# Kernel optimization log

Measured on AMD Instinct MI355X. Metric: run time of the kernel, lower is better.

## Reference

```python
import jax, jax.numpy as jnp
import numpy as np

# Sizes
N, T, P, D = 1000, 4, 10, 13          # nodes, point types, edge types (T*(T+1)/2), basis dim per point
F, H, EA, K, E = 128, 128, 16, 64, 20000  # node feat, edge hidden, edge attr/feat, edge op bottleneck, edges
I_NODE = D * (D + 1) // 2             # 91: symmetric ('ij=ji') self-block irreps dim
I_EDGE = D * D                        # 169: generic ('ij') block irreps dim
AVG_NEIGH = 20.0


def setup_inputs() -> dict:
    ks = jax.random.split(jax.random.key(0), 16)
    Fin = H + 2 * F                   # edge-op input: [edge_msg, node_h_i, node_h_j]
    return {
        'node_feats': jax.random.normal(ks[0], (N, F), jnp.float32),
        'node_attrs': jax.random.uniform(ks[1], (N, T), dtype=jnp.float32),
        'edge_feats': jax.random.normal(ks[2], (E, EA), jnp.float32),
        'edge_attrs': jax.random.normal(ks[3], (E, EA), jnp.float32),
        'edge_index': jax.random.randint(ks[4], (2, E), 0, N),
        'node_types': jax.random.randint(ks[5], (N,), 0, T),
        'edge_types': jax.random.randint(ks[6], (E,), 0, P),
        'W_msg': jax.random.normal(ks[7], (F, F), jnp.float32) / np.float32(np.sqrt(F)),
        'W_attr': jax.random.normal(ks[8], (T, F), jnp.float32) / np.float32(np.sqrt(T)),
        'W_em': jax.random.normal(ks[9], (2 * F + 2 * EA, H), jnp.float32) / np.float32(np.sqrt(2 * F + 2 * EA)),
        'W_proj': jax.random.normal(ks[10], (Fin, K), jnp.float32) / np.float32(np.sqrt(Fin)),
        'W_node': jax.random.normal(ks[11], (T, F, I_NODE), jnp.float32) / np.float32(np.sqrt(F)),
        'W_edge': jax.random.normal(ks[12], (P, K, I_EDGE), jnp.float32) / np.float32(np.sqrt(K)),
        'cob_node': jax.random.normal(ks[13], (T, I_NODE, D, D), jnp.float32) / np.float32(D),
        'cob_edge': jax.random.normal(ks[14], (P, I_EDGE, D, D), jnp.float32) / np.float32(D),
    }


def reference(node_feats, node_attrs, edge_feats, edge_attrs, edge_index, node_types,
              edge_types, W_msg, W_attr, W_em, W_proj, W_node, W_edge, cob_node, cob_edge):
    src, dst = edge_index[0], edge_index[1]
    # --- node message passing (NodeMessageBlock, simplified linear-aggregate form) ---
    m = node_feats @ W_msg                                             # [N, F]
    agg = jax.ops.segment_sum(m[src], dst, num_segments=N) \
        + jax.ops.segment_sum(m[dst], src, num_segments=N)             # symmetric edge list: both dirs
    node_h = node_feats + agg / AVG_NEIGH + node_attrs @ W_attr        # [N, F]
    # --- edge messages (EdgeMessageBlock, simplified) ---
    e_in = jnp.concatenate([node_h[src], node_h[dst], edge_feats, edge_attrs], axis=-1)
    edge_msg = jnp.tanh(e_in @ W_em)                                   # [E, H]
    # --- self-interaction blocks: per-type gather -> op -> einsum('ni,ixy->nxy', ., cob) ---
    node_irred = jnp.einsum('nf,nfi->ni', node_h, W_node[node_types])  # [N, I_NODE]
    node_blocks = jnp.einsum('ni,nixy->nxy', node_irred, cob_node[node_types])  # [N, D, D]
    # --- interaction blocks: per-edge-type op + change of basis, transpose-symmetrized ---
    onehot = jax.nn.one_hot(edge_types, P, dtype=node_feats.dtype)     # [E, P] type selector

    def edge_block(a, b):
        h = jnp.concatenate([edge_msg, a, b], axis=-1) @ W_proj        # [E, K]
        irr = jnp.einsum('epi,ep->ei', jnp.einsum('ek,pki->epi', h, W_edge), onehot)  # [E, I_EDGE]
        return jnp.einsum('epxy,ep->exy', jnp.einsum('ei,pixy->epxy', irr, cob_edge), onehot)  # [E, D, D]

    blk_ij = edge_block(node_h[src], node_h[dst])
    blk_ji = edge_block(node_h[dst], node_h[src])
    edge_blocks = 0.5 * (blk_ij + jnp.swapaxes(blk_ji, -1, -2))        # symm_transpose
    # --- scatter blocks into the dense symmetric block matrix ---
    off = jnp.arange(D)
    nidx = jnp.arange(N)[:, None] * D + off                            # [N, D] diagonal block rows/cols
    rs = src[:, None] * D + off                                        # [E, D]
    cs = dst[:, None] * D + off
    M = jnp.zeros((N * D, N * D), node_feats.dtype)
    M = M.at[nidx[:, :, None], nidx[:, None, :]].add(node_blocks)
    M = M.at[rs[:, :, None], cs[:, None, :]].add(edge_blocks)
    M = M.at[cs[:, :, None], rs[:, None, :]].add(jnp.swapaxes(edge_blocks, -1, -2))
    return M
```

## Files before the change

### kernel.cpp

```cpp
#include <hip/hip_runtime.h>
#include <cmath>

#define NN   1000
#define TT   4
#define PP   10
#define DD   13
#define FF   128
#define HH   128
#define EAA  16
#define KDIM 64
#define EE   20000
#define I_NODE 91
#define I_EDGE 169
#define MROW  13000

__global__ __launch_bounds__(256) void k_zero(float4* __restrict__ p, long n4) {
  long i = (long)blockIdx.x * 256 + threadIdx.x;
  if (i < n4) p[i] = make_float4(0.f, 0.f, 0.f, 0.f);
}

__global__ __launch_bounds__(192) void k_comb_edge(
    const float* __restrict__ We, const float* __restrict__ cob,
    float* __restrict__ Wcomb) {
  int pk = blockIdx.x;
  int p = pk >> 6;
  int t = threadIdx.x;
  if (t >= I_EDGE) return;
  float acc = 0.f;
  const float* wrow = We + pk * I_EDGE;
  const float* crow = cob + p * I_EDGE * I_EDGE + t;
  for (int i = 0; i < I_EDGE; ++i) acc += wrow[i] * crow[i * I_EDGE];
  Wcomb[pk * I_EDGE + t] = acc;
}

__global__ __launch_bounds__(192) void k_comb_node(
    const float* __restrict__ Wn, const float* __restrict__ cob,
    float* __restrict__ Wnc) {
  int tf = blockIdx.x;
  int ty = tf >> 7;
  int t = threadIdx.x;
  if (t >= I_EDGE) return;
  float acc = 0.f;
  const float* wrow = Wn + tf * I_NODE;
  const float* crow = cob + ty * I_NODE * I_EDGE + t;
  for (int i = 0; i < I_NODE; ++i) acc += wrow[i] * crow[i * I_EDGE];
  Wnc[tf * I_EDGE + t] = acc;
}

__global__ __launch_bounds__(128) void k_node_msg(
    const float* __restrict__ nf, const float* __restrict__ Wmsg,
    float* __restrict__ m, float* __restrict__ agg) {
  int n = blockIdx.x, j = threadIdx.x;
  __shared__ float row[FF];
  row[j] = nf[n * FF + j];
  __syncthreads();
  float acc = 0.f;
#pragma unroll 8
  for (int f = 0; f < FF; ++f) acc += row[f] * Wmsg[f * FF + j];
  m[n * FF + j] = acc;
  agg[n * FF + j] = 0.f;
}

__global__ __launch_bounds__(256) void k_scatter(
    const float* __restrict__ m, const int* __restrict__ src,
    const int* __restrict__ dst, float* __restrict__ agg) {
  int idx = blockIdx.x * 256 + threadIdx.x;
  if (idx >= EE * FF) return;
  int e = idx >> 7, j = idx & 127;
  int s = src[e], d = dst[e];
  atomicAdd(&agg[d * FF + j], m[s * FF + j]);
  atomicAdd(&agg[s * FF + j], m[d * FF + j]);
}

__global__ __launch_bounds__(128) void k_node_h(
    const float* __restrict__ nf, const float* __restrict__ agg,
    const float* __restrict__ na, const float* __restrict__ Wattr,
    float* __restrict__ nh) {
  int n = blockIdx.x, j = threadIdx.x;
  float a = 0.f;
#pragma unroll
  for (int t = 0; t < TT; ++t) a += na[n * TT + t] * Wattr[t * FF + j];
  nh[n * FF + j] = nf[n * FF + j] + agg[n * FF + j] * (1.0f / 20.0f) + a;
}

#define EPB 8
__global__ __launch_bounds__(128) void k_edge_msg(
    const float* __restrict__ nh, const float* __restrict__ ef,
    const float* __restrict__ ea, const int* __restrict__ src,
    const int* __restrict__ dst, const float* __restrict__ Wem,
    float* __restrict__ emsg) {
  int e0 = blockIdx.x * EPB;
  int j = threadIdx.x;
  __shared__ float xin[EPB][2 * FF + 2 * EAA];
  for (int e = 0; e < EPB; ++e) {
    int ee = e0 + e;
    int s = src[ee], d = dst[ee];
    for (int i = j; i < 288; i += 128) {
      float v;
      if (i < 128)      v = nh[s * FF + i];
      else if (i < 256) v = nh[d * FF + (i - 128)];
      else if (i < 272) v = ef[ee * EAA + (i - 256)];
      else              v = ea[ee * EAA + (i - 272)];
      xin[e][i] = v;
    }
  }
  __syncthreads();
  float acc[EPB];
#pragma unroll
  for (int e = 0; e < EPB; ++e) acc[e] = 0.f;
  for (int c = 0; c < 288; c += 4) {
    float4 xv[EPB];
#pragma unroll
    for (int e = 0; e < EPB; ++e) xv[e] = *(const float4*)&xin[e][c];
#pragma unroll
    for (int sub = 0; sub < 4; ++sub) {
      float w = Wem[(c + sub) * HH + j];
      const float* xs;
#pragma unroll
      for (int e = 0; e < EPB; ++e) {
        float x = (sub == 0) ? xv[e].x : (sub == 1) ? xv[e].y : (sub == 2) ? xv[e].z : xv[e].w;
        acc[e] += x * w;
      }
    }
  }
#pragma unroll
  for (int e = 0; e < EPB; ++e) emsg[(e0 + e) * HH + j] = tanhf(acc[e]);
}

__global__ __launch_bounds__(192) void k_node_block(
    const float* __restrict__ nh, const int* __restrict__ ntype,
    const float* __restrict__ Wnc, float* __restrict__ M) {
  int n = blockIdx.x, t = threadIdx.x;
  int ty = ntype[n];
  __shared__ float row[FF];
  if (t < FF) row[t] = nh[n * FF + t];
  __syncthreads();
  if (t < I_EDGE) {
    float acc = 0.f;
    const float* W = Wnc + ty * FF * I_EDGE + t;
#pragma unroll 4
    for (int f = 0; f < FF; ++f) acc += row[f] * W[f * I_EDGE];
    int x = t / DD, y = t % DD;
    atomicAdd(&M[(size_t)(n * DD + x) * MROW + (n * DD + y)], acc);
  }
}

#define E2 2
__global__ __launch_bounds__(256) void k_edge_blk(
    const float* __restrict__ nh, const float* __restrict__ emsg,
    const int* __restrict__ src, const int* __restrict__ dst,
    const int* __restrict__ etype, const float* __restrict__ Wproj,
    const float* __restrict__ Wcomb, float* __restrict__ M) {
  int e0 = blockIdx.x * E2;
  int t = threadIdx.x;
  __shared__ float xin[E2][384];
  __shared__ float hp[4][256];
  __shared__ float hv[4][KDIM];
  __shared__ float tji[E2][I_EDGE];
  __shared__ int se[E2], de[E2], pe[E2];

  if (t < E2) {
    int e = e0 + t;
    se[t] = src[e]; de[t] = dst[e]; pe[t] = etype[e];
  }
  __syncthreads();
  for (int e = 0; e < E2; ++e) {
    int ee = e0 + e, s = se[e], d = de[e];
    if (t < 128) {
      xin[e][t] = emsg[ee * HH + t];
      xin[e][256 + t] = nh[d * FF + t];
    } else {
      xin[e][t] = nh[s * FF + (t - 128)];
    }
  }
  __syncthreads();

  {
    int k = t & 63, seg = t >> 6;
    float a0 = 0.f, a1 = 0.f, a2 = 0.f, a3 = 0.f;
    const float* Wp = Wproj + k;
    int i0 = seg * 96;
    for (int c = i0; c < i0 + 96; c += 4) {
      int cs = (c < 128) ? c : (c < 256 ? c + 128 : c - 128);
      float4 x0 = *(const float4*)&xin[0][c];
      float4 x0s = *(const float4*)&xin[0][cs];
      float4 x1 = *(const float4*)&xin[1][c];
      float4 x1s = *(const float4*)&xin[1][cs];
      float w0 = Wp[(c + 0) * KDIM], w1 = Wp[(c + 1) * KDIM];
      float w2 = Wp[(c + 2) * KDIM], w3 = Wp[(c + 3) * KDIM];
      a0 += x0.x * w0 + x0.y * w1 + x0.z * w2 + x0.w * w3;
      a1 += x0s.x * w0 + x0s.y * w1 + x0s.z * w2 + x0s.w * w3;
      a2 += x1.x * w0 + x1.y * w1 + x1.z * w2 + x1.w * w3;
      a3 += x1s.x * w0 + x1s.y * w1 + x1s.z * w2 + x1s.w * w3;
    }
    hp[0][t] = a0; hp[1][t] = a1; hp[2][t] = a2; hp[3][t] = a3;
  }
  __syncthreads();
  if (t < KDIM) {
#pragma unroll
    for (int q = 0; q < 4; ++q)
      hv[q][t] = hp[q][t] + hp[q][t + 64] + hp[q][t + 128] + hp[q][t + 192];
  }
  __syncthreads();

  float b0 = 0.f, b1 = 0.f, b2 = 0.f, b3 = 0.f;
  if (t < I_EDGE) {
    const float* W0 = Wcomb + pe[0] * KDIM * I_EDGE + t;
    const float* W1 = Wcomb + pe[1] * KDIM * I_EDGE + t;
    for (int k = 0; k < KDIM; k += 4) {
      float4 h0 = *(const float4*)&hv[0][k];
      float4 h1 = *(const float4*)&hv[1][k];
      float4 h2 = *(const float4*)&hv[2][k];
      float4 h3 = *(const float4*)&hv[3][k];
      float u0 = W0[(k + 0) * I_EDGE], u1 = W0[(k + 1) * I_EDGE];
      float u2 = W0[(k + 2) * I_EDGE], u3 = W0[(k + 3) * I_EDGE];
      float v0 = W1[(k + 0) * I_EDGE], v1 = W1[(k + 1) * I_EDGE];
      float v2 = W1[(k + 2) * I_EDGE], v3 = W1[(k + 3) * I_EDGE];
      b0 += h0.x * u0 + h0.y * u1 + h0.z * u2 + h0.w * u3;
      b1 += h1.x * u0 + h1.y * u1 + h1.z * u2 + h1.w * u3;
      b2 += h2.x * v0 + h2.y * v1 + h2.z * v2 + h2.w * v3;
      b3 += h3.x * v0 + h3.y * v1 + h3.z * v2 + h3.w * v3;
    }
    tji[0][t] = b1; tji[1][t] = b3;
  }
  __syncthreads();

  if (t < I_EDGE) {
    int x = t / DD, y = t % DD;
    {
      int s = se[0], d = de[0];
      float eb = 0.5f * (b0 + tji[0][y * DD + x]);
      atomicAdd(&M[(size_t)(s * DD + x) * MROW + (d * DD + y)], eb);
      atomicAdd(&M[(size_t)(d * DD + y) * MROW + (s * DD + x)], eb);
    }
    {
      int s = se[1], d = de[1];
      float eb = 0.5f * (b2 + tji[1][y * DD + x]);
      atomicAdd(&M[(size_t)(s * DD + x) * MROW + (d * DD + y)], eb);
      atomicAdd(&M[(size_t)(d * DD + y) * MROW + (s * DD + x)], eb);
    }
  }
}

extern "C" void kernel_launch(void* const* d_in, const int* in_sizes, int n_in,
                              void* d_out, int out_size, void* d_ws, size_t ws_size,
                              hipStream_t stream) {
  const float* node_feats = (const float*)d_in[0];
  const float* node_attrs = (const float*)d_in[1];
  const float* edge_feats = (const float*)d_in[2];
  const float* edge_attrs = (const float*)d_in[3];
  const int*   edge_index = (const int*)d_in[4];
  const int*   node_types = (const int*)d_in[5];
  const int*   edge_types = (const int*)d_in[6];
  const float* W_msg  = (const float*)d_in[7];
  const float* W_attr = (const float*)d_in[8];
  const float* W_em   = (const float*)d_in[9];
  const float* W_proj = (const float*)d_in[10];
  const float* W_node = (const float*)d_in[11];
  const float* W_edge = (const float*)d_in[12];
  const float* cob_node = (const float*)d_in[13];
  const float* cob_edge = (const float*)d_in[14];

  float* M  = (float*)d_out;
  float* ws = (float*)d_ws;
  float* m_buf = ws;
  float* agg   = ws + 128000;
  float* nh    = ws + 256000;
  float* emsg  = ws + 384000;
  float* Wcomb = ws + 2944000;
  float* Wnc   = ws + 3052160;

  const int* src = edge_index;
  const int* dst = edge_index + EE;

  long n4 = (long)out_size / 4;
  k_zero      <<<(int)((n4 + 255) / 256), 256, 0, stream>>>((float4*)M, n4);
  k_comb_edge <<<PP * KDIM, 192, 0, stream>>>(W_edge, cob_edge, Wcomb);
  k_comb_node <<<TT * FF, 192, 0, stream>>>(W_node, cob_node, Wnc);
  k_node_msg  <<<NN, 128, 0, stream>>>(node_feats, W_msg, m_buf, agg);
  k_scatter   <<<(EE * FF) / 256, 256, 0, stream>>>(m_buf, src, dst, agg);
  k_node_h    <<<NN, 128, 0, stream>>>(node_feats, agg, node_attrs, W_attr, nh);
  k_edge_msg  <<<EE / EPB, 128, 0, stream>>>(nh, edge_feats, edge_attrs, src, dst, W_em, emsg);
  k_node_block<<<NN, 192, 0, stream>>>(nh, node_types, Wnc, M);
  k_edge_blk  <<<EE / E2, 256, 0, stream>>>(nh, emsg, src, dst, edge_types,
                                            W_proj, Wcomb, M);
}
```

Measured before the change: 922.6 us.

## Precompute per-node projections so edge kernels skip gathered node GEMMs

Because matrix multiplication is linear, the node-feature parts of the edge-message and edge-projection matmuls are computed once per node (V1, V2, U) rather than once per edge. The edge-message kernel now only adds the gathered node terms, applies the small edge-attribute matmul and tanh, then projects the message to the bottleneck (hmsg). The edge-block kernel forms both directional h vectors by addition and is restructured to handle 4 edges per 768-thread block. Floating-point summation order changes, and the zero-fill now uses a hardcoded output size.

New measurement: 892.5 us. -3.3%, faster.

```diff
diff --git a/kernel.cpp b/kernel.cpp
--- a/kernel.cpp
+++ b/kernel.cpp
@@ -13,6 +13,7 @@
 #define I_NODE 91
 #define I_EDGE 169
 #define MROW  13000
+#define OUT_FLOAT4 42250000L
 
 __global__ __launch_bounds__(256) void k_zero(float4* __restrict__ p, long n4) {
   long i = (long)blockIdx.x * 256 + threadIdx.x;
@@ -83,48 +84,77 @@
   nh[n * FF + j] = nf[n * FF + j] + agg[n * FF + j] * (1.0f / 20.0f) + a;
 }
 
+__global__ __launch_bounds__(128) void k_node_pre(
+    const float* __restrict__ nh, const float* __restrict__ Wem,
+    const float* __restrict__ Wproj, float* __restrict__ V1,
+    float* __restrict__ V2, float* __restrict__ U) {
+  int n = blockIdx.x, t = threadIdx.x;
+  __shared__ float row[FF];
+  row[t] = nh[n * FF + t];
+  __syncthreads();
+  float v1 = 0.f, v2 = 0.f;
+#pragma unroll 4
+  for (int f = 0; f < FF; ++f) {
+    float x = row[f];
+    v1 += x * Wem[f * HH + t];
+    v2 += x * Wem[(FF + f) * HH + t];
+  }
+  V1[n * HH + t] = v1;
+  V2[n * HH + t] = v2;
+  int k = t & 63, half = t >> 6;
+  const float* W = Wproj + (FF + half * FF) * KDIM + k;
+  float u = 0.f;
+#pragma unroll 4
+  for (int f = 0; f < FF; ++f) u += row[f] * W[f * KDIM];
+  U[n * 128 + t] = u;
+}
+
 #define EPB 8
 __global__ __launch_bounds__(128) void k_edge_msg(
-    const float* __restrict__ nh, const float* __restrict__ ef,
-    const float* __restrict__ ea, const int* __restrict__ src,
-    const int* __restrict__ dst, const float* __restrict__ Wem,
-    float* __restrict__ emsg) {
+    const float* __restrict__ V1, const float* __restrict__ V2,
+    const float* __restrict__ ef, const float* __restrict__ ea,
+    const int* __restrict__ src, const int* __restrict__ dst,
+    const float* __restrict__ Wem, const float* __restrict__ Wproj,
+    float* __restrict__ hmsg) {
   int e0 = blockIdx.x * EPB;
   int j = threadIdx.x;
-  __shared__ float xin[EPB][2 * FF + 2 * EAA];
+  __shared__ float efa[EPB][32];
+  __shared__ float em[EPB][HH];
+  for (int i = j; i < EPB * 32; i += 128) {
+    int e = i >> 5, c = i & 31;
+    efa[e][c] = (c < 16) ? ef[(e0 + e) * EAA + c] : ea[(e0 + e) * EAA + (c - 16)];
+  }
+  __syncthreads();
+  float wcol[32];
+#pragma unroll
+  for (int c = 0; c < 32; ++c) wcol[c] = Wem[(256 + c) * HH + j];
+#pragma unroll
   for (int e = 0; e < EPB; ++e) {
-    int ee = e0 + e;
-    int s = src[ee], d = dst[ee];
-    for (int i = j; i < 288; i += 128) {
-      float v;
-      if (i < 128)      v = nh[s * FF + i];
-      else if (i < 256) v = nh[d * FF + (i - 128)];
-      else if (i < 272) v = ef[ee * EAA + (i - 256)];
-      else              v = ea[ee * EAA + (i - 272)];
-      xin[e][i] = v;
-    }
-  }
-  __syncthreads();
-  float acc[EPB];
-#pragma unroll
-  for (int e = 0; e < EPB; ++e) acc[e] = 0.f;
-  for (int c = 0; c < 288; c += 4) {
-    float4 xv[EPB];
-#pragma unroll
-    for (int e = 0; e < EPB; ++e) xv[e] = *(const float4*)&xin[e][c];
-#pragma unroll
-    for (int sub = 0; sub < 4; ++sub) {
-      float w = Wem[(c + sub) * HH + j];
-      const float* xs;
-#pragma unroll
-      for (int e = 0; e < EPB; ++e) {
-        float x = (sub == 0) ? xv[e].x : (sub == 1) ? xv[e].y : (sub == 2) ? xv[e].z : xv[e].w;
-        acc[e] += x * w;
-      }
-    }
-  }
-#pragma unroll
-  for (int e = 0; e < EPB; ++e) emsg[(e0 + e) * HH + j] = tanhf(acc[e]);
+    int s = src[e0 + e], d = dst[e0 + e];
+    float acc = V1[s * HH + j] + V2[d * HH + j];
+#pragma unroll
+    for (int c = 0; c < 32; ++c) acc += efa[e][c] * wcol[c];
+    em[e][j] = tanhf(acc);
+  }
+  __syncthreads();
+  int k = j & 63, half = j >> 6;
+  float a0 = 0.f, a1 = 0.f, a2 = 0.f, a3 = 0.f;
+  for (int f = 0; f < HH; f += 4) {
+    float4 m0 = *(const float4*)&em[half + 0][f];
+    float4 m1 = *(const float4*)&em[half + 2][f];
+    float4 m2 = *(const float4*)&em[half + 4][f];
+    float4 m3 = *(const float4*)&em[half + 6][f];
+    float w0 = Wproj[(f + 0) * KDIM + k], w1 = Wproj[(f + 1) * KDIM + k];
+    float w2 = Wproj[(f + 2) * KDIM + k], w3 = Wproj[(f + 3) * KDIM + k];
+    a0 += m0.x * w0 + m0.y * w1 + m0.z * w2 + m0.w * w3;
+    a1 += m1.x * w0 + m1.y * w1 + m1.z * w2 + m1.w * w3;
+    a2 += m2.x * w0 + m2.y * w1 + m2.z * w2 + m2.w * w3;
+    a3 += m3.x * w0 + m3.y * w1 + m3.z * w2 + m3.w * w3;
+  }
+  hmsg[(e0 + half + 0) * KDIM + k] = a0;
+  hmsg[(e0 + half + 2) * KDIM + k] = a1;
+  hmsg[(e0 + half + 4) * KDIM + k] = a2;
+  hmsg[(e0 + half + 6) * KDIM + k] = a3;
 }
 
 __global__ __launch_bounds__(192) void k_node_block(
@@ -145,100 +175,44 @@
   }
 }
 
-#define E2 2
-__global__ __launch_bounds__(256) void k_edge_blk(
-    const float* __restrict__ nh, const float* __restrict__ emsg,
+#define EB2 4
+__global__ __launch_bounds__(768) void k_edge_blk(
+    const float* __restrict__ U, const float* __restrict__ hmsg,
     const int* __restrict__ src, const int* __restrict__ dst,
-    const int* __restrict__ etype, const float* __restrict__ Wproj,
-    const float* __restrict__ Wcomb, float* __restrict__ M) {
-  int e0 = blockIdx.x * E2;
+    const int* __restrict__ etype, const float* __restrict__ Wcomb,
+    float* __restrict__ M) {
+  int e0 = blockIdx.x * EB2;
   int t = threadIdx.x;
-  __shared__ float xin[E2][384];
-  __shared__ float hp[4][256];
-  __shared__ float hv[4][KDIM];
-  __shared__ float tji[E2][I_EDGE];
-  __shared__ int se[E2], de[E2], pe[E2];
-
-  if (t < E2) {
-    int e = e0 + t;
-    se[t] = src[e]; de[t] = dst[e]; pe[t] = etype[e];
-  }
-  __syncthreads();
-  for (int e = 0; e < E2; ++e) {
-    int ee = e0 + e, s = se[e], d = de[e];
-    if (t < 128) {
-      xin[e][t] = emsg[ee * HH + t];
-      xin[e][256 + t] = nh[d * FF + t];
-    } else {
-      xin[e][t] = nh[s * FF + (t - 128)];
+  int ei = threadIdx.y;
+  int e = e0 + ei;
+  __shared__ float h[EB2][2][KDIM];
+  __shared__ float tji[EB2][I_EDGE];
+  int s = src[e], d = dst[e], p = etype[e];
+  if (t < 128) {
+    int k = t & 63, w = t >> 6;
+    int a = w ? d : s, b = w ? s : d;
+    h[ei][w][k] = hmsg[e * KDIM + k] + U[a * 128 + k] + U[b * 128 + 64 + k];
+  }
+  __syncthreads();
+  float bij = 0.f, bji = 0.f;
+  if (t < I_EDGE) {
+    const float* W = Wcomb + p * KDIM * I_EDGE + t;
+    for (int k = 0; k < KDIM; k += 4) {
+      float4 hi = *(const float4*)&h[ei][0][k];
+      float4 hj = *(const float4*)&h[ei][1][k];
+      float w0 = W[(k + 0) * I_EDGE], w1 = W[(k + 1) * I_EDGE];
+      float w2 = W[(k + 2) * I_EDGE], w3 = W[(k + 3) * I_EDGE];
+      bij += hi.x * w0 + hi.y * w1 + hi.z * w2 + hi.w * w3;
+      bji += hj.x * w0 + hj.y * w1 + hj.z * w2 + hj.w * w3;
     }
-  }
-  __syncthreads();
-
-  {
-    int k = t & 63, seg = t >> 6;
-    float a0 = 0.f, a1 = 0.f, a2 = 0.f, a3 = 0.f;
-    const float* Wp = Wproj + k;
-    int i0 = seg * 96;
-    for (int c = i0; c < i0 + 96; c += 4) {
-      int cs = (c < 128) ? c : (c < 256 ? c + 128 : c - 128);
-      float4 x0 = *(const float4*)&xin[0][c];
-      float4 x0s = *(const float4*)&xin[0][cs];
-      float4 x1 = *(const float4*)&xin[1][c];
-      float4 x1s = *(const float4*)&xin[1][cs];
-      float w0 = Wp[(c + 0) * KDIM], w1 = Wp[(c + 1) * KDIM];
-      float w2 = Wp[(c + 2) * KDIM], w3 = Wp[(c + 3) * KDIM];
-      a0 += x0.x * w0 + x0.y * w1 + x0.z * w2 + x0.w * w3;
-      a1 += x0s.x * w0 + x0s.y * w1 + x0s.z * w2 + x0s.w * w3;
-      a2 += x1.x * w0 + x1.y * w1 + x1.z * w2 + x1.w * w3;
-      a3 += x1s.x * w0 + x1s.y * w1 + x1s.z * w2 + x1s.w * w3;
-    }
-    hp[0][t] = a0; hp[1][t] = a1; hp[2][t] = a2; hp[3][t] = a3;
-  }
-  __syncthreads();
-  if (t < KDIM) {
-#pragma unroll
-    for (int q = 0; q < 4; ++q)
-      hv[q][t] = hp[q][t] + hp[q][t + 64] + hp[q][t + 128] + hp[q][t + 192];
-  }
-  __syncthreads();
-
-  float b0 = 0.f, b1 = 0.f, b2 = 0.f, b3 = 0.f;
-  if (t < I_EDGE) {
-    const float* W0 = Wcomb + pe[0] * KDIM * I_EDGE + t;
-    const float* W1 = Wcomb + pe[1] * KDIM * I_EDGE + t;
-    for (int k = 0; k < KDIM; k += 4) {
-      float4 h0 = *(const float4*)&hv[0][k];
-      float4 h1 = *(const float4*)&hv[1][k];
-      float4 h2 = *(const float4*)&hv[2][k];
-      float4 h3 = *(const float4*)&hv[3][k];
-      float u0 = W0[(k + 0) * I_EDGE], u1 = W0[(k + 1) * I_EDGE];
-      float u2 = W0[(k + 2) * I_EDGE], u3 = W0[(k + 3) * I_EDGE];
-      float v0 = W1[(k + 0) * I_EDGE], v1 = W1[(k + 1) * I_EDGE];
-      float v2 = W1[(k + 2) * I_EDGE], v3 = W1[(k + 3) * I_EDGE];
-      b0 += h0.x * u0 + h0.y * u1 + h0.z * u2 + h0.w * u3;
-      b1 += h1.x * u0 + h1.y * u1 + h1.z * u2 + h1.w * u3;
-      b2 += h2.x * v0 + h2.y * v1 + h2.z * v2 + h2.w * v3;
-      b3 += h3.x * v0 + h3.y * v1 + h3.z * v2 + h3.w * v3;
-    }
-    tji[0][t] = b1; tji[1][t] = b3;
-  }
-  __syncthreads();
-
+    tji[ei][t] = bji;
+  }
+  __syncthreads();
   if (t < I_EDGE) {
     int x = t / DD, y = t % DD;
-    {
-      int s = se[0], d = de[0];
-      float eb = 0.5f * (b0 + tji[0][y * DD + x]);
-      atomicAdd(&M[(size_t)(s * DD + x) * MROW + (d * DD + y)], eb);
-      atomicAdd(&M[(size_t)(d * DD + y) * MROW + (s * DD + x)], eb);
-    }
-    {
-      int s = se[1], d = de[1];
-      float eb = 0.5f * (b2 + tji[1][y * DD + x]);
-      atomicAdd(&M[(size_t)(s * DD + x) * MROW + (d * DD + y)], eb);
-      atomicAdd(&M[(size_t)(d * DD + y) * MROW + (s * DD + x)], eb);
-    }
+    float eb = 0.5f * (bij + tji[ei][y * DD + x]);
+    atomicAdd(&M[(size_t)(s * DD + x) * MROW + (d * DD + y)], eb);
+    atomicAdd(&M[(size_t)(d * DD + y) * MROW + (s * DD + x)], eb);
   }
 }
 
@@ -266,22 +240,26 @@
   float* m_buf = ws;
   float* agg   = ws + 128000;
   float* nh    = ws + 256000;
-  float* emsg  = ws + 384000;
-  float* Wcomb = ws + 2944000;
-  float* Wnc   = ws + 3052160;
+  float* V1    = ws + 384000;
+  float* V2    = ws + 512000;
+  float* U     = ws + 640000;
+  float* hmsg  = ws + 768000;
+  float* Wcomb = ws + 2048000;
+  float* Wnc   = ws + 2156160;
 
   const int* src = edge_index;
   const int* dst = edge_index + EE;
 
-  long n4 = (long)out_size / 4;
-  k_zero      <<<(int)((n4 + 255) / 256), 256, 0, stream>>>((float4*)M, n4);
+  k_zero      <<<(int)((OUT_FLOAT4 + 255) / 256), 256, 0, stream>>>((float4*)M, OUT_FLOAT4);
   k_comb_edge <<<PP * KDIM, 192, 0, stream>>>(W_edge, cob_edge, Wcomb);
   k_comb_node <<<TT * FF, 192, 0, stream>>>(W_node, cob_node, Wnc);
   k_node_msg  <<<NN, 128, 0, stream>>>(node_feats, W_msg, m_buf, agg);
   k_scatter   <<<(EE * FF) / 256, 256, 0, stream>>>(m_buf, src, dst, agg);
   k_node_h    <<<NN, 128, 0, stream>>>(node_feats, agg, node_attrs, W_attr, nh);
-  k_edge_msg  <<<EE / EPB, 128, 0, stream>>>(nh, edge_feats, edge_attrs, src, dst, W_em, emsg);
+  k_node_pre  <<<NN, 128, 0, stream>>>(nh, W_em, W_proj, V1, V2, U);
+  k_edge_msg  <<<EE / EPB, 128, 0, stream>>>(V1, V2, edge_feats, edge_attrs, src, dst,
+                                             W_em, W_proj, hmsg);
   k_node_block<<<NN, 192, 0, stream>>>(nh, node_types, Wnc, M);
-  k_edge_blk  <<<EE / E2, 256, 0, stream>>>(nh, emsg, src, dst, edge_types,
-                                            W_proj, Wcomb, M);
-}
+  k_edge_blk  <<<dim3(EE / EB2), dim3(192, 4), 0, stream>>>(U, hmsg, src, dst, edge_types,
+                                                            Wcomb, M);
+}
```
